# Performance work log

Measured on AMD Instinct MI355X. Metric: run time of the kernel, lower is better.

Reference implementation:

```python
import jax, jax.numpy as jnp
import numpy as np

DS = 32   # self_obs_dim
DO = 32   # obstacle_obs_dim
D = DS + DO
H = 128   # obstacle_hidden_size
B = 512   # batch_size
A = 16    # num_adv_obs = 2 * num_oppo_obs


def _init_linear(key, fan_in, fan_out):
    kw, kb = jax.random.split(key)
    bound = 1.0 / np.sqrt(fan_in)
    w = jax.random.uniform(kw, (fan_in, fan_out), jnp.float32, -bound, bound)
    b = jax.random.uniform(kb, (fan_out,), jnp.float32, -bound, bound)
    return w, b


def setup_inputs() -> dict:
    key = jax.random.key(0)
    ks = jax.random.split(key, 10)
    obs = jax.random.normal(ks[0], (B, DS), jnp.float32)
    latent = jax.random.normal(ks[1], (B, A, DO), jnp.float32)
    hw1, hb1 = _init_linear(ks[2], D, H)
    hw2, hb2 = _init_linear(ks[3], H, D * H)
    vw1, vb1 = _init_linear(ks[4], H, H)
    vw2, vb2 = _init_linear(ks[5], H, H)
    aw1, ab1 = _init_linear(ks[6], 2 * H, H)
    aw2, ab2 = _init_linear(ks[7], H, H)
    aw3, ab3 = _init_linear(ks[8], H, 1)
    return {
        "obs": obs, "obs_intention_latent": latent,
        "hw1": hw1, "hb1": hb1, "hw2": hw2, "hb2": hb2,
        "vw1": vw1, "vb1": vb1, "vw2": vw2, "vb2": vb2,
        "aw1": aw1, "ab1": ab1, "aw2": aw2, "ab2": ab2,
        "aw3": aw3, "ab3": ab3,
        "num_adv_obs": A, "batch_size": B, "num_groups": 1,
    }


def reference(obs, obs_intention_latent, hw1, hb1, hw2, hb2,
              vw1, vb1, vw2, vb2, aw1, ab1, aw2, ab2, aw3, ab3,
              num_adv_obs, batch_size, num_groups):
    relu = jax.nn.relu
    # flatten opponents (batch-major, matches torch .reshape)
    obs_obstacles = obs_intention_latent.reshape(-1, DO)          # [N, DO]
    # torch .repeat(num_adv_obs, 1) tiles the batch dim
    self_rep = jnp.tile(obs[:, :DS], (num_adv_obs, 1))            # [N, DS]
    mlp_input = jnp.concatenate([self_rep, obs_obstacles], axis=1)  # [N, D]
    # hypernet: per-sample weight [N, D, H]
    h = relu(mlp_input @ hw1 + hb1)
    w = relu(h @ hw2 + hb2).reshape(-1, D, H)
    # per-sample vector-matrix product + tanh
    emb = jnp.tanh(jnp.einsum("nd,ndh->nh", mlp_input, w))        # [N, H]
    # neighbor value MLP
    vals = relu(relu(emb @ vw1 + vb1) @ vw2 + vb2)                # [N, H]
    # attention: concat with per-batch mean embedding
    emb_mean = jnp.mean(emb.reshape(batch_size, -1, H), axis=1)   # [B, H]
    mean_rep = jnp.tile(emb_mean, (num_adv_obs, 1))               # [N, H]
    att_in = jnp.concatenate([emb, mean_rep], axis=1)             # [N, 2H]
    scores = relu(relu(att_in @ aw1 + ab1) @ aw2 + ab2) @ aw3 + ab3  # [N, 1]
    att = jax.nn.softmax(scores.reshape(batch_size, -1), axis=1).reshape(-1, 1)
    weighted = (att * vals).reshape(batch_size, -1, H)
    return jnp.sum(weighted, axis=1)                              # [B, H]
```

## Files before the change

kernel.cpp:

```cpp
#include <hip/hip_runtime.h>
#include <hip/hip_bf16.h>
#include <math.h>

#define BATCH 512
#define NADV  16
#define NROWS (BATCH*NADV)
#define DS    32
#define DO    32
#define DIM   64
#define HID   128
#define WCOLS (DIM*HID)
#define LSTR  136
#define PACK_BLOCKS 276

typedef _Float16 half8 __attribute__((ext_vector_type(8)));
typedef float floatx4 __attribute__((ext_vector_type(4)));

__device__ inline void async_ld16(void* lds, const void* g) {
    __builtin_amdgcn_global_load_lds(
        (const __attribute__((address_space(1))) void*)g,
        (__attribute__((address_space(3))) void*)lds, 16, 0, 0);
}

__global__ __launch_bounds__(256)
void k_prep(const float* __restrict__ obs, const float* __restrict__ latent,
            const float* __restrict__ hw1, const float* __restrict__ hb1,
            const float* __restrict__ hw2, const float* __restrict__ vw1,
            const float* __restrict__ vw2, const float* __restrict__ aw1,
            const float* __restrict__ aw2,
            _Float16* __restrict__ hf,
            _Float16* __restrict__ w2p, _Float16* __restrict__ vw1p,
            _Float16* __restrict__ vw2p, _Float16* __restrict__ aw1p,
            _Float16* __restrict__ aw2p) {
    __shared__ __align__(16) float smem[32 * 132];
    int b = blockIdx.x;
    int tid = threadIdx.x;
    if (b < PACK_BLOCKS) {
        const float* src; _Float16* dst; int N, Kt, jb, kt;
        if (b < 256)      { src = hw2; dst = w2p;  N = WCOLS; Kt = 4; jb = b >> 2; kt = b & 3; }
        else if (b < 260) { src = vw1; dst = vw1p; N = HID;   Kt = 4; jb = 0; kt = b - 256; }
        else if (b < 264) { src = vw2; dst = vw2p; N = HID;   Kt = 4; jb = 0; kt = b - 260; }
        else if (b < 272) { src = aw1; dst = aw1p; N = HID;   Kt = 8; jb = 0; kt = b - 264; }
        else              { src = aw2; dst = aw2p; N = HID;   Kt = 4; jb = 0; kt = b - 272; }
        for (int i = tid; i < 32 * 32; i += 256) {
            int r = i >> 5, c4 = (i & 31) * 4;
            *(float4*)&smem[r * 132 + c4] =
                *(const float4*)(src + (size_t)(kt * 32 + r) * N + jb * 128 + c4);
        }
        __syncthreads();
        for (int i = tid; i < 8 * 64; i += 256) {
            int ctl = i >> 6, lane = i & 63;
            int ct = jb * 8 + ctl;
            int rbase = (lane >> 4) * 8, cc = ctl * 16 + (lane & 15);
            half8 v;
#pragma unroll
            for (int e = 0; e < 8; ++e) v[e] = (_Float16)smem[(rbase + e) * 132 + cc];
            *(half8*)(dst + ((size_t)ct * Kt + kt) * 512 + lane * 8) = v;
        }
    } else {
        int n0 = (b - PACK_BLOCKS) * 16;
        float* xs = smem;
        for (int idx = tid; idx < 16 * DIM; idx += 256) {
            int r = idx >> 6, d = idx & 63;
            int n = n0 + r;
            xs[r * DIM + d] = (d < DS) ? obs[(n & (BATCH - 1)) * DS + d]
                                       : latent[(size_t)n * DO + (d - DS)];
        }
        __syncthreads();
        int j = tid & 127, hh = tid >> 7;
        float acc[8];
        float bb = hb1[j];
#pragma unroll
        for (int r = 0; r < 8; ++r) acc[r] = bb;
        for (int d = 0; d < DIM; ++d) {
            float w = hw1[d * HID + j];
#pragma unroll
            for (int r = 0; r < 8; ++r)
                acc[r] = fmaf(xs[(hh * 8 + r) * DIM + d], w, acc[r]);
        }
#pragma unroll
        for (int r = 0; r < 8; ++r)
            hf[(size_t)(n0 + hh * 8 + r) * HID + j] = (_Float16)fmaxf(acc[r], 0.f);
    }
}

__global__ __launch_bounds__(512, 4)
void k_hyper_mfma(const float* __restrict__ obs, const float* __restrict__ latent,
                  const _Float16* __restrict__ hf, const _Float16* __restrict__ w2p,
                  const float* __restrict__ hb2,
                  _Float16* __restrict__ embf, _Float16* __restrict__ emeanf) {
    __shared__ __align__(16) _Float16 Bs[8][4][512];
    int b  = blockIdx.x;
    int jt = b & 7;
    int rt = b >> 3;
    int n0 = rt * 128;
    int j0 = jt * 16;
    int tid = threadIdx.x;
    int wave = tid >> 6, lane = tid & 63;
    int l15 = lane & 15, quad = lane >> 4;
    int row_lo = n0 + wave * 16 + quad * 4;

    half8 af[4];
    {
        const _Float16* arow = hf + (size_t)(n0 + wave * 16 + l15) * HID;
#pragma unroll
        for (int ks = 0; ks < 4; ++ks)
            af[ks] = *(const half8*)(arow + ks * 32 + quad * 8);
    }

    float emb_acc[4] = {0.f, 0.f, 0.f, 0.f};

#pragma unroll
    for (int d8 = 0; d8 < 8; ++d8) {
        {
            int ct = (d8 * 8 + wave) * 8 + jt;
            const _Float16* src = w2p + (size_t)ct * 2048 + lane * 8;
            _Float16* dst = &Bs[wave][0][0];
#pragma unroll
            for (int kt = 0; kt < 4; ++kt)
                async_ld16(dst + kt * 512, src + kt * 512);
        }
        __syncthreads();

        float xr[4][8];
#pragma unroll
        for (int r = 0; r < 4; ++r) {
            int row = row_lo + r;
            const float* p = (d8 < 4)
                ? obs + (size_t)(row & (BATCH - 1)) * DS + d8 * 8
                : latent + (size_t)row * DO + (d8 - 4) * 8;
            float4 t0 = *(const float4*)p;
            float4 t1 = *(const float4*)(p + 4);
            xr[r][0] = t0.x; xr[r][1] = t0.y; xr[r][2] = t0.z; xr[r][3] = t0.w;
            xr[r][4] = t1.x; xr[r][5] = t1.y; xr[r][6] = t1.z; xr[r][7] = t1.w;
        }

#pragma unroll
        for (int dd = 0; dd < 8; ++dd) {
            int d = d8 * 8 + dd;
            float bb = hb2[d * HID + j0 + l15];
            floatx4 acc = {bb, bb, bb, bb};
#pragma unroll
            for (int ks = 0; ks < 4; ++ks) {
                half8 bfr = *(const half8*)&Bs[dd][ks][lane * 8];
                acc = __builtin_amdgcn_mfma_f32_16x16x32_f16(af[ks], bfr, acc, 0, 0, 0);
            }
#pragma unroll
            for (int reg = 0; reg < 4; ++reg)
                emb_acc[reg] = fmaf(xr[reg][dd], fmaxf(acc[reg], 0.f), emb_acc[reg]);
        }
        __syncthreads();
    }

    float e[4];
#pragma unroll
    for (int reg = 0; reg < 4; ++reg) {
        e[reg] = tanhf(emb_acc[reg]);
        embf[(size_t)(n0 + wave * 16 + quad * 4 + reg) * HID + j0 + l15] =
            (_Float16)e[reg];
    }
    float s = e[0] + e[1] + e[2] + e[3];
    s += __shfl_xor(s, 16, 64);
    s += __shfl_xor(s, 32, 64);
    if (quad == 0)
        emeanf[(size_t)(rt * 8 + wave) * HID + j0 + l15] = (_Float16)(s * (1.f / 16));
}

__global__ __launch_bounds__(512, 4)
void k_tail(const _Float16* __restrict__ embf, const _Float16* __restrict__ emeanf,
            const _Float16* __restrict__ vw1p, const float* __restrict__ vb1,
            const _Float16* __restrict__ vw2p, const float* __restrict__ vb2,
            const _Float16* __restrict__ aw1p, const float* __restrict__ ab1,
            const _Float16* __restrict__ aw2p, const float* __restrict__ ab2,
            const float* __restrict__ aw3, const float* __restrict__ ab3,
            float* __restrict__ out) {
    __shared__ _Float16 tAs[16][LSTR];
    __shared__ _Float16 tBs[16][LSTR];
    __shared__ _Float16 tCs[16][LSTR];
    __shared__ float att[16];
    int g = blockIdx.x;
    int n0 = g * 16;
    int tid = threadIdx.x;
    int wave = tid >> 6, lane = tid & 63, l15 = lane & 15, quad = lane >> 4;
    int ct = wave;

    half8 av[4], amean[4];
    {
        const _Float16* erow = embf + (size_t)(n0 + l15) * HID;
        const _Float16* mrow = emeanf + (size_t)((n0 + l15) & (BATCH - 1)) * HID;
#pragma unroll
        for (int ks = 0; ks < 4; ++ks) {
            av[ks]    = *(const half8*)(erow + ks * 32 + quad * 8);
            amean[ks] = *(const half8*)(mrow + ks * 32 + quad * 8);
        }
    }

    floatx4 acc;
    {
        float bb = vb1[ct * 16 + l15];
        acc = (floatx4){bb, bb, bb, bb};
    }
#pragma unroll
    for (int ks = 0; ks < 4; ++ks) {
        half8 bfr = *(const half8*)(vw1p + ((size_t)ct * 4 + ks) * 512 + lane * 8);
        acc = __builtin_amdgcn_mfma_f32_16x16x32_f16(av[ks], bfr, acc, 0, 0, 0);
    }
#pragma unroll
    for (int reg = 0; reg < 4; ++reg)
        tAs[quad * 4 + reg][ct * 16 + l15] = (_Float16)fmaxf(acc[reg], 0.f);
    __syncthreads();

    half8 at[4];
#pragma unroll
    for (int ks = 0; ks < 4; ++ks)
        at[ks] = *(const half8*)&tAs[l15][ks * 32 + quad * 8];

    floatx4 vacc;
    {
        float bb = vb2[ct * 16 + l15];
        vacc = (floatx4){bb, bb, bb, bb};
    }
#pragma unroll
    for (int ks = 0; ks < 4; ++ks) {
        half8 bfr = *(const half8*)(vw2p + ((size_t)ct * 4 + ks) * 512 + lane * 8);
        vacc = __builtin_amdgcn_mfma_f32_16x16x32_f16(at[ks], bfr, vacc, 0, 0, 0);
    }

    floatx4 aacc;
    {
        float bb = ab1[ct * 16 + l15];
        aacc = (floatx4){bb, bb, bb, bb};
    }
#pragma unroll
    for (int ks = 0; ks < 8; ++ks) {
        half8 bfr = *(const half8*)(aw1p + ((size_t)ct * 8 + ks) * 512 + lane * 8);
        half8 a = (ks < 4) ? av[ks] : amean[ks - 4];
        aacc = __builtin_amdgcn_mfma_f32_16x16x32_f16(a, bfr, aacc, 0, 0, 0);
    }
#pragma unroll
    for (int reg = 0; reg < 4; ++reg)
        tBs[quad * 4 + reg][ct * 16 + l15] = (_Float16)fmaxf(aacc[reg], 0.f);
    __syncthreads();

    half8 aa[4];
#pragma unroll
    for (int ks = 0; ks < 4; ++ks)
        aa[ks] = *(const half8*)&tBs[l15][ks * 32 + quad * 8];

    floatx4 a2acc;
    {
        float bb = ab2[ct * 16 + l15];
        a2acc = (floatx4){bb, bb, bb, bb};
    }
#pragma unroll
    for (int ks = 0; ks < 4; ++ks) {
        half8 bfr = *(const half8*)(aw2p + ((size_t)ct * 4 + ks) * 512 + lane * 8);
        a2acc = __builtin_amdgcn_mfma_f32_16x16x32_f16(aa[ks], bfr, a2acc, 0, 0, 0);
    }
#pragma unroll
    for (int reg = 0; reg < 4; ++reg)
        tCs[quad * 4 + reg][ct * 16 + l15] = (_Float16)fmaxf(a2acc[reg], 0.f);
    __syncthreads();

    if (wave == 0) {
        int r = lane >> 2, q4 = lane & 3;
        float p = 0.f;
#pragma unroll
        for (int c = 0; c < 4; ++c) {
            half8 v = *(const half8*)&tCs[r][q4 * 32 + c * 8];
            float4 w0 = *(const float4*)(aw3 + q4 * 32 + c * 8);
            float4 w1 = *(const float4*)(aw3 + q4 * 32 + c * 8 + 4);
            p += (float)v[0] * w0.x + (float)v[1] * w0.y +
                 (float)v[2] * w0.z + (float)v[3] * w0.w +
                 (float)v[4] * w1.x + (float)v[5] * w1.y +
                 (float)v[6] * w1.z + (float)v[7] * w1.w;
        }
        p += __shfl_xor(p, 1, 64);
        p += __shfl_xor(p, 2, 64);
        float s = p + ab3[0];
        float m = s;
#pragma unroll
        for (int off = 4; off < 64; off <<= 1) m = fmaxf(m, __shfl_xor(m, off, 64));
        float e = expf(s - m);
        float S = e;
#pragma unroll
        for (int off = 4; off < 64; off <<= 1) S += __shfl_xor(S, off, 64);
        if (q4 == 0) att[r] = e / S;
    }
    __syncthreads();

    {
        float p = 0.f;
#pragma unroll
        for (int reg = 0; reg < 4; ++reg)
            p += att[quad * 4 + reg] * fmaxf(vacc[reg], 0.f);
        p += __shfl_xor(p, 16, 64);
        p += __shfl_xor(p, 32, 64);
        if (quad == 0) out[(size_t)g * HID + ct * 16 + l15] = p;
    }
}

extern "C" void kernel_launch(void* const* d_in, const int* in_sizes, int n_in,
                              void* d_out, int out_size, void* d_ws, size_t ws_size,
                              hipStream_t stream) {
    const float* obs = (const float*)d_in[0];
    const float* lat = (const float*)d_in[1];
    const float* hw1 = (const float*)d_in[2];
    const float* hb1 = (const float*)d_in[3];
    const float* hw2 = (const float*)d_in[4];
    const float* hb2 = (const float*)d_in[5];
    const float* vw1 = (const float*)d_in[6];
    const float* vb1 = (const float*)d_in[7];
    const float* vw2 = (const float*)d_in[8];
    const float* vb2 = (const float*)d_in[9];
    const float* aw1 = (const float*)d_in[10];
    const float* ab1 = (const float*)d_in[11];
    const float* aw2 = (const float*)d_in[12];
    const float* ab2 = (const float*)d_in[13];
    const float* aw3 = (const float*)d_in[14];
    const float* ab3 = (const float*)d_in[15];
    float* out = (float*)d_out;

    char* ws = (char*)d_ws;
    _Float16*  hf     = (_Float16*)ws;  ws += (size_t)NROWS * HID * 2;
    _Float16*  w2p    = (_Float16*)ws;  ws += (size_t)WCOLS * HID * 2;
    _Float16*  embf   = (_Float16*)ws;  ws += (size_t)NROWS * HID * 2;
    _Float16*  emeanf = (_Float16*)ws;  ws += (size_t)BATCH * HID * 2;
    _Float16*  vw1p   = (_Float16*)ws;  ws += (size_t)HID * HID * 2;
    _Float16*  vw2p   = (_Float16*)ws;  ws += (size_t)HID * HID * 2;
    _Float16*  aw1p   = (_Float16*)ws;  ws += (size_t)2 * HID * HID * 2;
    _Float16*  aw2p   = (_Float16*)ws;  ws += (size_t)HID * HID * 2;

    hipLaunchKernelGGL(k_prep, dim3(PACK_BLOCKS + NROWS / 16), dim3(256), 0, stream,
                       obs, lat, hw1, hb1, hw2, vw1, vw2, aw1, aw2,
                       hf, w2p, vw1p, vw2p, aw1p, aw2p);
    hipLaunchKernelGGL(k_hyper_mfma, dim3(512), dim3(512), 0, stream,
                       obs, lat, hf, w2p, hb2, embf, emeanf);
    hipLaunchKernelGGL(k_tail, dim3(BATCH), dim3(512), 0, stream,
                       embf, emeanf, vw1p, vb1, vw2p, vb2,
                       aw1p, ab1, aw2p, ab2, aw3, ab3, out);
}
```

Baseline: 136.4 us.

## Fuse first hypernet layer into hyper MFMA kernel via LDS

The first hypernetwork layer (input @ hw1 + relu) moves out of the prep kernel and into k_hyper_mfma. It is now computed with MFMA from a packed fp16 hw1 and written to LDS, where it becomes the A operand. This removes the hf workspace round trip through global memory and the scalar FMA blocks in k_prep, which now only packs weights. The cost is that each of the 8 column-tile blocks per row tile recomputes the same h rows, adds two block barriers, and rounds the inputs to fp16.

```diff
diff --git a/kernel.cpp b/kernel.cpp
--- a/kernel.cpp
+++ b/kernel.cpp
@@ -11,7 +11,7 @@
 #define HID   128
 #define WCOLS (DIM*HID)
 #define LSTR  136
-#define PACK_BLOCKS 276
+#define PACK_BLOCKS 278
 
 typedef _Float16 half8 __attribute__((ext_vector_type(8)));
 typedef float floatx4 __attribute__((ext_vector_type(4)));
@@ -23,73 +23,47 @@
 }
 
 __global__ __launch_bounds__(256)
-void k_prep(const float* __restrict__ obs, const float* __restrict__ latent,
-            const float* __restrict__ hw1, const float* __restrict__ hb1,
-            const float* __restrict__ hw2, const float* __restrict__ vw1,
-            const float* __restrict__ vw2, const float* __restrict__ aw1,
-            const float* __restrict__ aw2,
-            _Float16* __restrict__ hf,
-            _Float16* __restrict__ w2p, _Float16* __restrict__ vw1p,
-            _Float16* __restrict__ vw2p, _Float16* __restrict__ aw1p,
-            _Float16* __restrict__ aw2p) {
+void k_prep(const float* __restrict__ hw1, const float* __restrict__ hw2,
+            const float* __restrict__ vw1, const float* __restrict__ vw2,
+            const float* __restrict__ aw1, const float* __restrict__ aw2,
+            _Float16* __restrict__ hw1p, _Float16* __restrict__ w2p,
+            _Float16* __restrict__ vw1p, _Float16* __restrict__ vw2p,
+            _Float16* __restrict__ aw1p, _Float16* __restrict__ aw2p) {
     __shared__ __align__(16) float smem[32 * 132];
     int b = blockIdx.x;
     int tid = threadIdx.x;
-    if (b < PACK_BLOCKS) {
-        const float* src; _Float16* dst; int N, Kt, jb, kt;
-        if (b < 256)      { src = hw2; dst = w2p;  N = WCOLS; Kt = 4; jb = b >> 2; kt = b & 3; }
-        else if (b < 260) { src = vw1; dst = vw1p; N = HID;   Kt = 4; jb = 0; kt = b - 256; }
-        else if (b < 264) { src = vw2; dst = vw2p; N = HID;   Kt = 4; jb = 0; kt = b - 260; }
-        else if (b < 272) { src = aw1; dst = aw1p; N = HID;   Kt = 8; jb = 0; kt = b - 264; }
-        else              { src = aw2; dst = aw2p; N = HID;   Kt = 4; jb = 0; kt = b - 272; }
-        for (int i = tid; i < 32 * 32; i += 256) {
-            int r = i >> 5, c4 = (i & 31) * 4;
-            *(float4*)&smem[r * 132 + c4] =
-                *(const float4*)(src + (size_t)(kt * 32 + r) * N + jb * 128 + c4);
-        }
-        __syncthreads();
-        for (int i = tid; i < 8 * 64; i += 256) {
-            int ctl = i >> 6, lane = i & 63;
-            int ct = jb * 8 + ctl;
-            int rbase = (lane >> 4) * 8, cc = ctl * 16 + (lane & 15);
-            half8 v;
-#pragma unroll
-            for (int e = 0; e < 8; ++e) v[e] = (_Float16)smem[(rbase + e) * 132 + cc];
-            *(half8*)(dst + ((size_t)ct * Kt + kt) * 512 + lane * 8) = v;
-        }
-    } else {
-        int n0 = (b - PACK_BLOCKS) * 16;
-        float* xs = smem;
-        for (int idx = tid; idx < 16 * DIM; idx += 256) {
-            int r = idx >> 6, d = idx & 63;
-            int n = n0 + r;
-            xs[r * DIM + d] = (d < DS) ? obs[(n & (BATCH - 1)) * DS + d]
-                                       : latent[(size_t)n * DO + (d - DS)];
-        }
-        __syncthreads();
-        int j = tid & 127, hh = tid >> 7;
-        float acc[8];
-        float bb = hb1[j];
-#pragma unroll
-        for (int r = 0; r < 8; ++r) acc[r] = bb;
-        for (int d = 0; d < DIM; ++d) {
-            float w = hw1[d * HID + j];
-#pragma unroll
-            for (int r = 0; r < 8; ++r)
-                acc[r] = fmaf(xs[(hh * 8 + r) * DIM + d], w, acc[r]);
-        }
-#pragma unroll
-        for (int r = 0; r < 8; ++r)
-            hf[(size_t)(n0 + hh * 8 + r) * HID + j] = (_Float16)fmaxf(acc[r], 0.f);
+    const float* src; _Float16* dst; int N, Kt, jb, kt;
+    if (b < 256)      { src = hw2; dst = w2p;  N = WCOLS; Kt = 4; jb = b >> 2; kt = b & 3; }
+    else if (b < 260) { src = vw1; dst = vw1p; N = HID;   Kt = 4; jb = 0; kt = b - 256; }
+    else if (b < 264) { src = vw2; dst = vw2p; N = HID;   Kt = 4; jb = 0; kt = b - 260; }
+    else if (b < 272) { src = aw1; dst = aw1p; N = HID;   Kt = 8; jb = 0; kt = b - 264; }
+    else if (b < 276) { src = aw2; dst = aw2p; N = HID;   Kt = 4; jb = 0; kt = b - 272; }
+    else              { src = hw1; dst = hw1p; N = HID;   Kt = 2; jb = 0; kt = b - 276; }
+    for (int i = tid; i < 32 * 32; i += 256) {
+        int r = i >> 5, c4 = (i & 31) * 4;
+        *(float4*)&smem[r * 132 + c4] =
+            *(const float4*)(src + (size_t)(kt * 32 + r) * N + jb * 128 + c4);
+    }
+    __syncthreads();
+    for (int i = tid; i < 8 * 64; i += 256) {
+        int ctl = i >> 6, lane = i & 63;
+        int ct = jb * 8 + ctl;
+        int rbase = (lane >> 4) * 8, cc = ctl * 16 + (lane & 15);
+        half8 v;
+#pragma unroll
+        for (int e = 0; e < 8; ++e) v[e] = (_Float16)smem[(rbase + e) * 132 + cc];
+        *(half8*)(dst + ((size_t)ct * Kt + kt) * 512 + lane * 8) = v;
     }
 }
 
 __global__ __launch_bounds__(512, 4)
 void k_hyper_mfma(const float* __restrict__ obs, const float* __restrict__ latent,
-                  const _Float16* __restrict__ hf, const _Float16* __restrict__ w2p,
-                  const float* __restrict__ hb2,
+                  const _Float16* __restrict__ hw1p, const float* __restrict__ hb1,
+                  const _Float16* __restrict__ w2p, const float* __restrict__ hb2,
                   _Float16* __restrict__ embf, _Float16* __restrict__ emeanf) {
-    __shared__ __align__(16) _Float16 Bs[8][4][512];
+    __shared__ __align__(16) char lds_raw[128 * LSTR * 2];
+    _Float16 (*hs)[LSTR] = (_Float16(*)[LSTR])lds_raw;
+    _Float16* Bs = (_Float16*)lds_raw;
     int b  = blockIdx.x;
     int jt = b & 7;
     int rt = b >> 3;
@@ -100,13 +74,45 @@
     int l15 = lane & 15, quad = lane >> 4;
     int row_lo = n0 + wave * 16 + quad * 4;
 
+    {
+        int row = n0 + wave * 16 + l15;
+        half8 ax[2];
+        {
+            const float* p0 = obs + (size_t)(row & (BATCH - 1)) * DS + quad * 8;
+            const float* p1 = latent + (size_t)row * DO + quad * 8;
+            float4 a0 = *(const float4*)p0, b0 = *(const float4*)(p0 + 4);
+            float4 a1 = *(const float4*)p1, b1 = *(const float4*)(p1 + 4);
+            ax[0][0] = (_Float16)a0.x; ax[0][1] = (_Float16)a0.y;
+            ax[0][2] = (_Float16)a0.z; ax[0][3] = (_Float16)a0.w;
+            ax[0][4] = (_Float16)b0.x; ax[0][5] = (_Float16)b0.y;
+            ax[0][6] = (_Float16)b0.z; ax[0][7] = (_Float16)b0.w;
+            ax[1][0] = (_Float16)a1.x; ax[1][1] = (_Float16)a1.y;
+            ax[1][2] = (_Float16)a1.z; ax[1][3] = (_Float16)a1.w;
+            ax[1][4] = (_Float16)b1.x; ax[1][5] = (_Float16)b1.y;
+            ax[1][6] = (_Float16)b1.z; ax[1][7] = (_Float16)b1.w;
+        }
+#pragma unroll
+        for (int ct2 = 0; ct2 < 8; ++ct2) {
+            float bb = hb1[ct2 * 16 + l15];
+            floatx4 hacc = {bb, bb, bb, bb};
+#pragma unroll
+            for (int ks2 = 0; ks2 < 2; ++ks2) {
+                half8 bfr = *(const half8*)(hw1p + ((size_t)ct2 * 2 + ks2) * 512 + lane * 8);
+                hacc = __builtin_amdgcn_mfma_f32_16x16x32_f16(ax[ks2], bfr, hacc, 0, 0, 0);
+            }
+#pragma unroll
+            for (int reg = 0; reg < 4; ++reg)
+                hs[wave * 16 + quad * 4 + reg][ct2 * 16 + l15] =
+                    (_Float16)fmaxf(hacc[reg], 0.f);
+        }
+    }
+    __syncthreads();
+
     half8 af[4];
-    {
-        const _Float16* arow = hf + (size_t)(n0 + wave * 16 + l15) * HID;
-#pragma unroll
-        for (int ks = 0; ks < 4; ++ks)
-            af[ks] = *(const half8*)(arow + ks * 32 + quad * 8);
-    }
+#pragma unroll
+    for (int ks = 0; ks < 4; ++ks)
+        af[ks] = *(const half8*)&hs[wave * 16 + l15][ks * 32 + quad * 8];
+    __syncthreads();
 
     float emb_acc[4] = {0.f, 0.f, 0.f, 0.f};
 
@@ -115,7 +121,7 @@
         {
             int ct = (d8 * 8 + wave) * 8 + jt;
             const _Float16* src = w2p + (size_t)ct * 2048 + lane * 8;
-            _Float16* dst = &Bs[wave][0][0];
+            _Float16* dst = Bs + (size_t)wave * 2048;
 #pragma unroll
             for (int kt = 0; kt < 4; ++kt)
                 async_ld16(dst + kt * 512, src + kt * 512);
@@ -142,7 +148,7 @@
             floatx4 acc = {bb, bb, bb, bb};
 #pragma unroll
             for (int ks = 0; ks < 4; ++ks) {
-                half8 bfr = *(const half8*)&Bs[dd][ks][lane * 8];
+                half8 bfr = *(const half8*)(Bs + ((size_t)dd * 4 + ks) * 512 + lane * 8);
                 acc = __builtin_amdgcn_mfma_f32_16x16x32_f16(af[ks], bfr, acc, 0, 0, 0);
             }
 #pragma unroll
@@ -322,20 +328,20 @@
     float* out = (float*)d_out;
 
     char* ws = (char*)d_ws;
-    _Float16*  hf     = (_Float16*)ws;  ws += (size_t)NROWS * HID * 2;
     _Float16*  w2p    = (_Float16*)ws;  ws += (size_t)WCOLS * HID * 2;
     _Float16*  embf   = (_Float16*)ws;  ws += (size_t)NROWS * HID * 2;
     _Float16*  emeanf = (_Float16*)ws;  ws += (size_t)BATCH * HID * 2;
+    _Float16*  hw1p   = (_Float16*)ws;  ws += (size_t)DIM * HID * 2;
     _Float16*  vw1p   = (_Float16*)ws;  ws += (size_t)HID * HID * 2;
     _Float16*  vw2p   = (_Float16*)ws;  ws += (size_t)HID * HID * 2;
     _Float16*  aw1p   = (_Float16*)ws;  ws += (size_t)2 * HID * HID * 2;
     _Float16*  aw2p   = (_Float16*)ws;  ws += (size_t)HID * HID * 2;
 
-    hipLaunchKernelGGL(k_prep, dim3(PACK_BLOCKS + NROWS / 16), dim3(256), 0, stream,
-                       obs, lat, hw1, hb1, hw2, vw1, vw2, aw1, aw2,
-                       hf, w2p, vw1p, vw2p, aw1p, aw2p);
+    hipLaunchKernelGGL(k_prep, dim3(PACK_BLOCKS), dim3(256), 0, stream,
+                       hw1, hw2, vw1, vw2, aw1, aw2,
+                       hw1p, w2p, vw1p, vw2p, aw1p, aw2p);
     hipLaunchKernelGGL(k_hyper_mfma, dim3(512), dim3(512), 0, stream,
-                       obs, lat, hf, w2p, hb2, embf, emeanf);
+                       obs, lat, hw1p, hb1, w2p, hb2, embf, emeanf);
     hipLaunchKernelGGL(k_tail, dim3(BATCH), dim3(512), 0, stream,
                        embf, emeanf, vw1p, vb1, vw2p, vb2,
                        aw1p, ab1, aw2p, ab2, aw3, ab3, out);
```

Result: faster. 133.2 us (-2.4%).
